# Kernel tuning notes

Hardware: AMD Instinct MI355X
Metric: run time of the kernel (lower is better)

## Reference

```python
import jax, jax.numpy as jnp
import numpy as np

MIN_DIST = 32  # minimum_extrema_distance from init_kwargs


def _extrema_mask(x):
    # x: [L]. Matches torch: dx padded with 0 on right (>0) and left (<=0);
    # sign = (1 - sign(x)).bool() is True iff x <= 0.
    dx = x[1:] - x[:-1]
    right = jnp.pad(dx, (0, 1)) > 0        # rising on the right
    left = jnp.pad(dx, (1, 0)) <= 0        # non-rising on the left
    neg = x <= 0
    valleys = right & left & neg
    peaks = (~right) & (~left) & (~neg)
    return valleys | peaks


def _suppress(x):
    # Greedy NMS-like suppression over one sample. x: [L]
    L = x.shape[0]
    e = _extrema_mask(x)
    # Sort ALL positions by |x| descending, with non-extrema pushed to the end
    key = jnp.where(e, jnp.abs(x), -jnp.inf)
    order = jnp.argsort(-key)              # candidate j -> original index order[j]
    valid = e[order]                       # which sorted candidates are real extrema
    idx = order                            # original positions, in sorted order

    def step(sec, i):
        # If candidate i not yet suppressed: suppress all candidates within
        # MIN_DIST of its position, then un-suppress itself.
        cond = jnp.logical_not(sec[i])
        window = (idx >= idx[i] - MIN_DIST) & (idx <= idx[i] + MIN_DIST)
        new_sec = jnp.where(cond, (sec | window).at[i].set(False), sec)
        return new_sec, None

    sec0 = jnp.logical_not(valid)          # non-extrema start suppressed
    sec, _ = jax.lax.scan(step, sec0, jnp.arange(L))
    primary_sorted = valid & jnp.logical_not(sec)
    # scatter back to original positions (order is a permutation)
    primary = jnp.zeros((L,), dtype=bool).at[order].set(primary_sorted)
    return jnp.where(primary, x, jnp.zeros_like(x))


def setup_inputs() -> dict:
    key = jax.random.key(0)
    input_ = jax.random.normal(key, (128, 1, 4096), dtype=jnp.float32)
    return {"input_": input_}


def reference(input_):
    x = input_[:, 0, :]                    # [B, L]
    out = jax.vmap(_suppress)(x)           # [B, L]
    return out[:, None, :]                 # [B, 1, L]
```

## Files before the change

kernel.cpp:

```cpp
#include <hip/hip_runtime.h>

#define L 4096
#define NT 256
#define C 16
#define NC (NT + 4)
#define SS 20
#define KSUB 2

typedef unsigned int u32;
typedef unsigned long long u64;

static __device__ __forceinline__ u32 umax(u32 a, u32 b) { return a > b ? a : b; }


#define RESCAN()                                                         \
    do {                                                                 \
        u32 pf_[C], sf_[C];                                              \
        u32 p_ = 0, nom_ = 0;                                            \
        _Pragma("unroll")                                                \
        for (int o_ = 0; o_ < C; ++o_) {                                 \
            u32 k_ = key[o_];                                            \
            if (k_ > p_) { p_ = k_; nom_ = (u32)o_; }                    \
            pf_[o_] = p_;                                                \
        }                                                                \
        u32 s_ = 0;                                                      \
        _Pragma("unroll")                                                \
        for (int o_ = C - 1; o_ >= 0; --o_) {                            \
            s_ = umax(s_, key[o_]); sf_[o_] = s_;                        \
        }                                                                \
        u32* pr_ = &pfxS[cc * SS];                                       \
        u32* sr_ = &sfxS[cc * SS];                                       \
        _Pragma("unroll")                                                \
        for (int q_ = 0; q_ < C; q_ += 4) {                              \
            *reinterpret_cast<uint4*>(pr_ + q_) =                        \
                make_uint4(pf_[q_], pf_[q_+1], pf_[q_+2], pf_[q_+3]);    \
            *reinterpret_cast<uint4*>(sr_ + q_) =                        \
                make_uint4(sf_[q_], sf_[q_+1], sf_[q_+2], sf_[q_+3]);    \
        }                                                                \
        TAc[cc] = p_;                                                    \
        run = p_; om = nom_;                                             \
    } while (0)

#define ZERO_SCANS()                                                     \
    do {                                                                 \
        uint4 z_ = make_uint4(0, 0, 0, 0);                               \
        u32* pr_ = &pfxS[cc * SS];                                       \
        u32* sr_ = &sfxS[cc * SS];                                       \
        _Pragma("unroll")                                                \
        for (int q_ = 0; q_ < C; q_ += 4) {                              \
            *reinterpret_cast<uint4*>(pr_ + q_) = z_;                    \
            *reinterpret_cast<uint4*>(sr_ + q_) = z_;                    \
        }                                                                \
        TAc[cc] = 0;                                                     \
    } while (0)

__global__ __launch_bounds__(NT) void extrema_nms_kernel(const float* __restrict__ in,
                                                         float* __restrict__ out) {
    __shared__ u32 pfxS[NC * SS];
    __shared__ u32 sfxS[NC * SS];
    __shared__ u32 TAc[NC];
    __shared__ u32 winC[NC];
    __shared__ u32 lastChange;

    const int tid = threadIdx.x;
    const int cc = tid + 2;
    const int base = tid * C;
    const float* xrow = in + (size_t)blockIdx.x * L;

    if (tid < 4 * SS) {
        int rsel = tid / SS;
        int row = (rsel & 1) + ((rsel >> 1) ? (NT + 2) : 0);
        int col = tid % SS;
        pfxS[row * SS + col] = 0;
        sfxS[row * SS + col] = 0;
    }
    if (tid < 4) {
        int slot = (tid & 1) + ((tid >> 1) ? (NT + 2) : 0);
        TAc[slot] = 0;
        winC[slot] = 0;
    }
    winC[cc] = 0;
    if (tid == 0) lastChange = 0;

    float xv[C];
    #pragma unroll
    for (int k = 0; k < C; k += 4) {
        float4 f = *reinterpret_cast<const float4*>(xrow + base + k);
        xv[k] = f.x; xv[k + 1] = f.y; xv[k + 2] = f.z; xv[k + 3] = f.w;
    }
    float xl = (base > 0) ? xrow[base - 1] : 0.0f;
    float xr = (base + C < L) ? xrow[base + C] : 0.0f;

    u32 key[C];
    #pragma unroll
    for (int o = 0; o < C; ++o) {
        int i = base + o;
        float xi = xv[o];
        float xp = (o == 0) ? xl : xv[o - 1];
        float xn = (o == C - 1) ? xr : xv[o + 1];
        bool right = (i < L - 1) && (xn > xi);
        bool left  = (i == 0) || (xi <= xp);
        bool neg   = (xi <= 0.0f);
        bool ext = (right && left && neg) || (!right && !left && !neg);
        key[o] = ext ? ((__float_as_uint(xi) & 0x7fffffffu) + 1u) : 0u;
    }

    u32 alivem = 0;
    #pragma unroll
    for (int o = 0; o < C; ++o) if (key[o]) alivem |= (1u << o);
    u32 run, om;
    RESCAN();
    u32 keptm = 0;
    u64 appliedW0 = 0;
    u32 appliedW1 = 0;
    __syncthreads();

    for (int r = 1; r <= 200; ++r) {
        bool changedAny = false;
        #pragma unroll
        for (int s = 0; s < KSUB; ++s) {
            if (run) {
                u32 m0 = winC[cc - 2], m1 = winC[cc - 1];
                u32 m3 = winC[cc + 1], m4 = winC[cc + 2];
                u32 sL = sfxS[(cc - 2) * SS + om];
                u32 tL = TAc[cc - 1];
                u32 tR = TAc[cc + 1];
                u32 pR = pfxS[(cc + 2) * SS + om];

                u64 W0 = (u64)m0 | ((u64)m1 << 16) | ((u64)m3 << 48);
                u32 W1 = m4;
                bool omChanged = false;
                if ((W0 ^ appliedW0) | (u64)(W1 ^ appliedW1)) {
                    appliedW0 = W0; appliedW1 = W1;
                    u32 supmask = 0;
                    if (W0) { int h0 = 63 - __clzll(W0);
                              supmask = (h0 >= 15) ? 0xffffu : ((2u << h0) - 1u); }
                    if (W1) { int l1 = __ffs((int)W1) - 1;
                              supmask |= ~((1u << l1) - 1u); }
                    u32 nA = alivem & ~supmask;
                    if (nA != alivem) {
                        alivem = nA;
                        changedAny = true;
                        if (nA == 0) {
                            ZERO_SCANS();
                            run = 0;
                        } else {
                            #pragma unroll
                            for (int o = 0; o < C; ++o)
                                key[o] = ((supmask >> o) & 1u) ? 0u : key[o];
                            RESCAN();
                            omChanged = true;
                        }
                    }
                }

                if (run) {
                    if (omChanged) {
                        sL = sfxS[(cc - 2) * SS + om];
                        pR = pfxS[(cc + 2) * SS + om];
                    }
                    u32 bL = umax(sL, tL);
                    u32 bR = umax(tR, pR);
                    if (bL < run && bR <= run) {
                        keptm |= 1u << om;
                        winC[cc] = 1u << om;
                        changedAny = true;
                        ZERO_SCANS();
                        run = 0; alivem = 0;
                    }
                }
            }
        }
        if (changedAny) lastChange = r;
        __syncthreads();
        if (lastChange < (u32)r) break;
    }

    float* orow = out + (size_t)blockIdx.x * L;
    #pragma unroll
    for (int k = 0; k < C; k += 4) {
        float4 f;
        f.x = ((keptm >> (k + 0)) & 1u) ? xv[k + 0] : 0.0f;
        f.y = ((keptm >> (k + 1)) & 1u) ? xv[k + 1] : 0.0f;
        f.z = ((keptm >> (k + 2)) & 1u) ? xv[k + 2] : 0.0f;
        f.w = ((keptm >> (k + 3)) & 1u) ? xv[k + 3] : 0.0f;
        *reinterpret_cast<float4*>(orow + base + k) = f;
    }
}

extern "C" void kernel_launch(void* const* d_in, const int* in_sizes, int n_in,
                              void* d_out, int out_size, void* d_ws, size_t ws_size,
                              hipStream_t stream) {
    const float* in = (const float*)d_in[0];
    float* out = (float*)d_out;
    int rows = in_sizes[0] / L;
    extrema_nms_kernel<<<rows, NT, 0, stream>>>(in, out);
}
```

Baseline: 14.32 us.

## Replace barrier-synchronized rounds with barrier-free asynchronous LDS polling loop

Removes the per-round __syncthreads and lastChange bookkeeping, so threads iterate independently and read neighbor state through volatile shared-memory accesses, with explicit lgkmcnt fences after writes. A wave exits once its ballot shows no thread is still running, and a re-check of neighbor windows before committing a keep guards against races. The aim is to cut barrier cost and let fast regions converge without waiting on the whole block. In exchange, cross-wave visibility now relies on volatile LDS ordering, and waves can spin on stale data, so correctness and convergence become timing dependent.

```diff
diff --git a/kernel.cpp b/kernel.cpp
--- a/kernel.cpp
+++ b/kernel.cpp
@@ -5,53 +5,66 @@
 #define C 16
 #define NC (NT + 4)
 #define SS 20
-#define KSUB 2
+#define MAXIT 30000
 
 typedef unsigned int u32;
 typedef unsigned long long u64;
 
 static __device__ __forceinline__ u32 umax(u32 a, u32 b) { return a > b ? a : b; }
 
-
-#define RESCAN()                                                         \
-    do {                                                                 \
-        u32 pf_[C], sf_[C];                                              \
-        u32 p_ = 0, nom_ = 0;                                            \
-        _Pragma("unroll")                                                \
-        for (int o_ = 0; o_ < C; ++o_) {                                 \
-            u32 k_ = key[o_];                                            \
-            if (k_ > p_) { p_ = k_; nom_ = (u32)o_; }                    \
-            pf_[o_] = p_;                                                \
-        }                                                                \
-        u32 s_ = 0;                                                      \
-        _Pragma("unroll")                                                \
-        for (int o_ = C - 1; o_ >= 0; --o_) {                            \
-            s_ = umax(s_, key[o_]); sf_[o_] = s_;                        \
-        }                                                                \
-        u32* pr_ = &pfxS[cc * SS];                                       \
-        u32* sr_ = &sfxS[cc * SS];                                       \
-        _Pragma("unroll")                                                \
-        for (int q_ = 0; q_ < C; q_ += 4) {                              \
-            *reinterpret_cast<uint4*>(pr_ + q_) =                        \
-                make_uint4(pf_[q_], pf_[q_+1], pf_[q_+2], pf_[q_+3]);    \
-            *reinterpret_cast<uint4*>(sr_ + q_) =                        \
-                make_uint4(sf_[q_], sf_[q_+1], sf_[q_+2], sf_[q_+3]);    \
-        }                                                                \
-        TAc[cc] = p_;                                                    \
-        run = p_; om = nom_;                                             \
+#define LDS_FENCE() asm volatile("s_waitcnt lgkmcnt(0)" ::: "memory")
+
+#define RESCAN()                                                          \
+    do {                                                                  \
+        u32* pr_ = &pfxS[cc * SS];                                        \
+        u32* sr_ = &sfxS[cc * SS];                                        \
+        u32 p_ = 0, nom_ = 0;                                             \
+        _Pragma("unroll")                                                 \
+        for (int g_ = 0; g_ < C; g_ += 4) {                               \
+            u32 t0_, t1_, t2_, t3_, k_;                                   \
+            k_ = key[g_+0]; if (k_ > p_) { p_ = k_; nom_ = g_+0; } t0_ = p_; \
+            k_ = key[g_+1]; if (k_ > p_) { p_ = k_; nom_ = g_+1; } t1_ = p_; \
+            k_ = key[g_+2]; if (k_ > p_) { p_ = k_; nom_ = g_+2; } t2_ = p_; \
+            k_ = key[g_+3]; if (k_ > p_) { p_ = k_; nom_ = g_+3; } t3_ = p_; \
+            *reinterpret_cast<uint4*>(pr_ + g_) = make_uint4(t0_,t1_,t2_,t3_); \
+        }                                                                 \
+        u32 s_ = 0;                                                       \
+        _Pragma("unroll")                                                 \
+        for (int g_ = C - 4; g_ >= 0; g_ -= 4) {                          \
+            u32 t3_ = umax(s_, key[g_+3]);                                \
+            u32 t2_ = umax(t3_, key[g_+2]);                               \
+            u32 t1_ = umax(t2_, key[g_+1]);                               \
+            u32 t0_ = umax(t1_, key[g_+0]);                               \
+            *reinterpret_cast<uint4*>(sr_ + g_) = make_uint4(t0_,t1_,t2_,t3_); \
+            s_ = t0_;                                                     \
+        }                                                                 \
+        TAc[cc] = p_;                                                     \
+        run = p_; om = nom_;                                              \
     } while (0)
 
-#define ZERO_SCANS()                                                     \
-    do {                                                                 \
-        uint4 z_ = make_uint4(0, 0, 0, 0);                               \
-        u32* pr_ = &pfxS[cc * SS];                                       \
-        u32* sr_ = &sfxS[cc * SS];                                       \
-        _Pragma("unroll")                                                \
-        for (int q_ = 0; q_ < C; q_ += 4) {                              \
-            *reinterpret_cast<uint4*>(pr_ + q_) = z_;                    \
-            *reinterpret_cast<uint4*>(sr_ + q_) = z_;                    \
-        }                                                                \
-        TAc[cc] = 0;                                                     \
+#define ZERO_SCANS()                                                      \
+    do {                                                                  \
+        uint4 z_ = make_uint4(0,0,0,0);                                   \
+        u32* pr_ = &pfxS[cc * SS];                                        \
+        u32* sr_ = &sfxS[cc * SS];                                        \
+        _Pragma("unroll")                                                 \
+        for (int q_ = 0; q_ < C; q_ += 4) {                               \
+            *reinterpret_cast<uint4*>(pr_ + q_) = z_;                     \
+            *reinterpret_cast<uint4*>(sr_ + q_) = z_;                     \
+        }                                                                 \
+        TAc[cc] = 0;                                                      \
+    } while (0)
+
+#define SUPMASK_OF(mm0, mm1, mm3, mm4, dst)                               \
+    do {                                                                  \
+        u64 w0_ = (u64)(mm0) | ((u64)(mm1) << 16) | ((u64)(mm3) << 48);   \
+        u32 w1_ = (mm4);                                                  \
+        u32 sm_ = 0;                                                      \
+        if (w0_) { int h_ = 63 - __clzll(w0_);                            \
+                   sm_ = (h_ >= 15) ? 0xffffu : ((2u << h_) - 1u); }      \
+        if (w1_) { int l_ = __ffs((int)w1_) - 1;                          \
+                   sm_ |= ~((1u << l_) - 1u); }                           \
+        (dst) = sm_ & 0xffffu;                                            \
     } while (0)
 
 __global__ __launch_bounds__(NT) void extrema_nms_kernel(const float* __restrict__ in,
@@ -60,7 +73,11 @@
     __shared__ u32 sfxS[NC * SS];
     __shared__ u32 TAc[NC];
     __shared__ u32 winC[NC];
-    __shared__ u32 lastChange;
+
+    volatile u32* const vpfx = pfxS;
+    volatile u32* const vsfx = sfxS;
+    volatile u32* const vTA  = TAc;
+    volatile u32* const vwin = winC;
 
     const int tid = threadIdx.x;
     const int cc = tid + 2;
@@ -80,7 +97,6 @@
         winC[slot] = 0;
     }
     winC[cc] = 0;
-    if (tid == 0) lastChange = 0;
 
     float xv[C];
     #pragma unroll
@@ -111,69 +127,61 @@
     u32 run, om;
     RESCAN();
     u32 keptm = 0;
+    __syncthreads();
+
     u64 appliedW0 = 0;
     u32 appliedW1 = 0;
-    __syncthreads();
-
-    for (int r = 1; r <= 200; ++r) {
-        bool changedAny = false;
-        #pragma unroll
-        for (int s = 0; s < KSUB; ++s) {
-            if (run) {
-                u32 m0 = winC[cc - 2], m1 = winC[cc - 1];
-                u32 m3 = winC[cc + 1], m4 = winC[cc + 2];
-                u32 sL = sfxS[(cc - 2) * SS + om];
-                u32 tL = TAc[cc - 1];
-                u32 tR = TAc[cc + 1];
-                u32 pR = pfxS[(cc + 2) * SS + om];
-
-                u64 W0 = (u64)m0 | ((u64)m1 << 16) | ((u64)m3 << 48);
-                u32 W1 = m4;
-                bool omChanged = false;
-                if ((W0 ^ appliedW0) | (u64)(W1 ^ appliedW1)) {
-                    appliedW0 = W0; appliedW1 = W1;
-                    u32 supmask = 0;
-                    if (W0) { int h0 = 63 - __clzll(W0);
-                              supmask = (h0 >= 15) ? 0xffffu : ((2u << h0) - 1u); }
-                    if (W1) { int l1 = __ffs((int)W1) - 1;
-                              supmask |= ~((1u << l1) - 1u); }
-                    u32 nA = alivem & ~supmask;
-                    if (nA != alivem) {
-                        alivem = nA;
-                        changedAny = true;
-                        if (nA == 0) {
-                            ZERO_SCANS();
-                            run = 0;
-                        } else {
-                            #pragma unroll
-                            for (int o = 0; o < C; ++o)
-                                key[o] = ((supmask >> o) & 1u) ? 0u : key[o];
-                            RESCAN();
-                            omChanged = true;
-                        }
+    for (int it = 0; it < MAXIT; ++it) {
+        if (__ballot(run != 0) == 0) break;
+        if (run) {
+            u32 m0 = vwin[cc - 2], m1 = vwin[cc - 1];
+            u32 m3 = vwin[cc + 1], m4 = vwin[cc + 2];
+            u32 sL = vsfx[(cc - 2) * SS + (int)om];
+            u32 tL = vTA[cc - 1], tR = vTA[cc + 1];
+            u32 pR = vpfx[(cc + 2) * SS + (int)om];
+
+            u64 W0 = (u64)m0 | ((u64)m1 << 16) | ((u64)m3 << 48);
+            u32 W1 = m4;
+            if (W0 != appliedW0 || W1 != appliedW1) {
+                appliedW0 = W0; appliedW1 = W1;
+                u32 supmask; SUPMASK_OF(m0, m1, m3, m4, supmask);
+                u32 nA = alivem & ~supmask;
+                if (nA != alivem) {
+                    alivem = nA;
+                    if (nA == 0) {
+                        ZERO_SCANS();
+                        run = 0;
+                        LDS_FENCE();
+                    } else {
+                        #pragma unroll
+                        for (int o = 0; o < C; ++o)
+                            key[o] = ((supmask >> o) & 1u) ? 0u : key[o];
+                        RESCAN();
+                        LDS_FENCE();
+                        sL = vsfx[(cc - 2) * SS + (int)om];
+                        tL = vTA[cc - 1]; tR = vTA[cc + 1];
+                        pR = vpfx[(cc + 2) * SS + (int)om];
                     }
                 }
-
-                if (run) {
-                    if (omChanged) {
-                        sL = sfxS[(cc - 2) * SS + om];
-                        pR = pfxS[(cc + 2) * SS + om];
-                    }
-                    u32 bL = umax(sL, tL);
-                    u32 bR = umax(tR, pR);
-                    if (bL < run && bR <= run) {
+            }
+            if (run) {
+                u32 bL = umax(sL, tL);
+                u32 bR = umax(tR, pR);
+                if (bL < run && bR <= run) {
+                    u32 n0 = vwin[cc - 2], n1 = vwin[cc - 1];
+                    u32 n3 = vwin[cc + 1], n4 = vwin[cc + 2];
+                    u32 sup2; SUPMASK_OF(n0, n1, n3, n4, sup2);
+                    if (!((sup2 >> om) & 1u)) {
                         keptm |= 1u << om;
-                        winC[cc] = 1u << om;
-                        changedAny = true;
+                        vwin[cc] = 1u << om;
+                        LDS_FENCE();
                         ZERO_SCANS();
                         run = 0; alivem = 0;
+                        LDS_FENCE();
                     }
                 }
             }
         }
-        if (changedAny) lastChange = r;
-        __syncthreads();
-        if (lastChange < (u32)r) break;
     }
 
     float* orow = out + (size_t)blockIdx.x * L;
```

Result: slower. 17.28 us (+20.6%).
